# Optimization experiments

Measured on AMD Instinct MI355X. Metric: run time of the kernel, lower is better.

Reference implementation:

```python
import jax, jax.numpy as jnp
import numpy as np

K = 20          # neighbors
EPS = 1e-5      # BatchNorm eps
SLOPE = 0.2     # LeakyReLU negative slope


def setup_inputs() -> dict:
    key = jax.random.key(0)
    ks = jax.random.split(key, 6)
    B, C, N, O = 8, 3, 4096, 64
    x = jax.random.normal(ks[0], (B, C, N), dtype=jnp.float32)
    W = jax.random.normal(ks[1], (O, 2 * C), dtype=jnp.float32) * 0.1  # conv1x1 weight, bias=False
    gamma = 1.0 + 0.1 * jax.random.normal(ks[2], (O,), dtype=jnp.float32)
    beta = 0.1 * jax.random.normal(ks[3], (O,), dtype=jnp.float32)
    mean = 0.1 * jax.random.normal(ks[4], (O,), dtype=jnp.float32)
    var = jax.random.uniform(ks[5], (O,), dtype=jnp.float32, minval=0.5, maxval=1.5)
    return {"x": x, "W": W, "gamma": gamma, "beta": beta, "mean": mean, "var": var}


def reference(x, W, gamma, beta, mean, var):
    # x: [B, C, N]
    B, C, N = x.shape
    xt = jnp.swapaxes(x, 1, 2)                                   # [B, N, C]
    xx = jnp.sum(x * x, axis=1)                                  # [B, N]
    pd = 2.0 * jnp.einsum('bnc,bmc->bnm', xt, xt) - xx[:, :, None] - xx[:, None, :]
    _, idx = jax.lax.top_k(pd, K)                                # [B, N, K] nearest neighbors
    # gather neighbor features per batch
    feat = jax.vmap(lambda f, i: f[i])(xt, idx)                  # [B, N, K, C]
    center = xt[:, :, None, :]                                   # [B, N, 1, C]
    edge = jnp.concatenate(
        [feat - center, jnp.broadcast_to(center, feat.shape)], axis=-1)  # [B, N, K, 2C]
    # 1x1 conv == channel matmul
    y = jnp.einsum('bnkc,oc->bnko', edge, W)                     # [B, N, K, O]
    inv = gamma / jnp.sqrt(var + EPS)                            # fused inference BatchNorm
    y = y * inv + (beta - mean * inv)
    y = jnp.where(y >= 0, y, SLOPE * y)                          # LeakyReLU(0.2)
    y = jnp.max(y, axis=2)                                       # max over k -> [B, N, O]
    return jnp.swapaxes(y, 1, 2)                                 # [B, O, N]
```

## Files before the change

kernel.cpp:

```cpp
#include <hip/hip_runtime.h>
#include <math.h>

#define NPTS 4096
#define KNN  20
#define NOUT 64
#define QPB  8
#define BLKT (QPB * 64)
#define PCAP 128
#define HALF 2048

__device__ __forceinline__ unsigned ord32(float f) {
    unsigned u = __float_as_uint(f);
    int m = ((int)u) >> 31;
    return u ^ ((unsigned)m | 0x80000000u);
}

__device__ __forceinline__ int mbcnt64(unsigned long long m) {
    return __builtin_amdgcn_mbcnt_hi((unsigned)(m >> 32),
           __builtin_amdgcn_mbcnt_lo((unsigned)m, 0));
}

__global__ __launch_bounds__(256) void pack_kernel(const float* __restrict__ x,
                                                   float4* __restrict__ xq) {
    const int i = blockIdx.x * 256 + threadIdx.x;
    const int b = i >> 12, j = i & (NPTS - 1);
    const float* xb = x + (size_t)b * 3 * NPTS;
    const float a0 = xb[j], a1 = xb[NPTS + j], a2 = xb[2 * NPTS + j];
    xq[i] = make_float4(a0, a1, a2, -fmaf(a0, a0, fmaf(a1, a1, a2 * a2)));
}

__global__ __launch_bounds__(BLKT, 6) void edgeconv_kernel(
    const float4* __restrict__ xq,
    const float* __restrict__ Wm,
    const float* __restrict__ gamma,
    const float* __restrict__ beta,
    const float* __restrict__ mean,
    const float* __restrict__ var,
    float* __restrict__ out)
{
    const int bid = blockIdx.x;
    const int b   = bid >> 9;
    const int n0  = (bid & 511) * QPB;
    const int t    = threadIdx.x;
    const int lane = t & 63;
    const int w    = t >> 6;

    __shared__ float4 tile[HALF];
    __shared__ unsigned long long pool[QPB * PCAP];
    __shared__ unsigned idxs[QPB][KNN];
    __shared__ float outT[NOUT * 9];
    __shared__ int cnt[QPB];

    const float4* xqb = xq + (size_t)b * NPTS;

    if (lane == 0) cnt[w] = 0;

    #pragma unroll
    for (int k2 = 0; k2 < HALF / BLKT; ++k2) {
        const int c = t + k2 * BLKT;
        tile[c] = xqb[c];
    }
    __syncthreads();

    const int nu = __builtin_amdgcn_readfirstlane(n0 + w);
    const float4 pv = xqb[nu];
    const float q0 = 2.f * pv.x, q1 = 2.f * pv.y, q2 = 2.f * pv.z;

    float vmax = -INFINITY;
    #pragma unroll
    for (int g = 0; g < 4; ++g) {
        float4 cc[8];
        #pragma unroll
        for (int u = 0; u < 8; ++u) cc[u] = tile[(g * 8 + u) * 64 + lane];
        #pragma unroll
        for (int u = 0; u < 8; ++u) {
            const float e = fmaf(q0, cc[u].x, fmaf(q1, cc[u].y, fmaf(q2, cc[u].z, cc[u].w)));
            vmax = fmaxf(vmax, e);
        }
    }

    float T;
    {
        float v = vmax;
        #pragma unroll
        for (int k = 2; k <= 64; k <<= 1) {
            #pragma unroll
            for (int j = k >> 1; j > 0; j >>= 1) {
                const float o = __shfl_xor(v, j, 64);
                const bool keep_min = ((lane & j) == 0) == ((lane & k) != 0);
                v = keep_min ? fminf(v, o) : fmaxf(v, o);
            }
        }
        T = __shfl(v, 19, 64);
    }

    const int invl = (NPTS - 1) - lane;
    #pragma unroll
    for (int g = 0; g < 4; ++g) {
        float4 cc[8];
        #pragma unroll
        for (int u = 0; u < 8; ++u) cc[u] = tile[(g * 8 + u) * 64 + lane];
        #pragma unroll
        for (int u = 0; u < 8; ++u) {
            const float e = fmaf(q0, cc[u].x, fmaf(q1, cc[u].y, fmaf(q2, cc[u].z, cc[u].w)));
            if (e >= T) {
                const int pos = atomicAdd(&cnt[w], 1);
                if (pos < PCAP)
                    pool[w * PCAP + pos] =
                        ((unsigned long long)ord32(e) << 32) |
                        (unsigned)(invl - (g * 8 + u) * 64);
            }
        }
    }

    #pragma unroll
    for (int g = 4; g < 8; ++g) {
        float4 cc[8];
        #pragma unroll
        for (int u = 0; u < 8; ++u) cc[u] = xqb[(g * 8 + u) * 64 + lane];
        #pragma unroll
        for (int u = 0; u < 8; ++u) {
            const float e = fmaf(q0, cc[u].x, fmaf(q1, cc[u].y, fmaf(q2, cc[u].z, cc[u].w)));
            if (e >= T) {
                const int pos = atomicAdd(&cnt[w], 1);
                if (pos < PCAP)
                    pool[w * PCAP + pos] =
                        ((unsigned long long)ord32(e) << 32) |
                        (unsigned)(invl - (g * 8 + u) * 64);
            }
        }
    }

    const int cntw = __builtin_amdgcn_readfirstlane(cnt[w]);
    const int cnt_ = (cntw < PCAP) ? cntw : PCAP;

    unsigned long long kk = 0ull;
    if (lane < cnt_) kk = pool[w * PCAP + lane];

    if (cnt_ <= 64) {
        const unsigned key = (unsigned)(kk >> 32);
        unsigned v = key;
        #pragma unroll
        for (int k = 2; k <= 64; k <<= 1) {
            #pragma unroll
            for (int j = k >> 1; j > 0; j >>= 1) {
                const unsigned o = (unsigned)__shfl_xor((int)v, j, 64);
                const bool keep_min = ((lane & j) == 0) == ((lane & k) != 0);
                v = keep_min ? min(v, o) : max(v, o);
            }
        }
        const unsigned K20 = (unsigned)__shfl((int)v, 19, 64);
        const unsigned long long ge = __ballot(key >= K20);
        if (__popcll(ge) == KNN) {
            if (key >= K20) idxs[w][mbcnt64(ge)] = (unsigned)kk;
        } else {
            unsigned long long key64 = kk;
            #pragma unroll
            for (int k = 2; k <= 64; k <<= 1) {
                #pragma unroll
                for (int j = k >> 1; j > 0; j >>= 1) {
                    const unsigned long long o = __shfl_xor(key64, j, 64);
                    const bool keep_min = ((lane & j) == 0) == ((lane & k) != 0);
                    const unsigned long long mn = (key64 < o) ? key64 : o;
                    const unsigned long long mx = (key64 < o) ? o : key64;
                    key64 = keep_min ? mn : mx;
                }
            }
            if (lane < KNN) idxs[w][lane] = (unsigned)key64;
        }
    } else {
        for (int r = 0; r < KNN; ++r) {
            unsigned long long bk = 0ull; int bp = -1;
            for (int i = lane; i < cnt_; i += 64) {
                const unsigned long long e = pool[w * PCAP + i];
                if (e > bk) { bk = e; bp = i; }
            }
            unsigned long long rb = bk;
            #pragma unroll
            for (int s = 32; s > 0; s >>= 1) {
                const unsigned long long o = __shfl_xor(rb, s, 64);
                if (o > rb) rb = o;
            }
            if (bk == rb && bp >= 0) pool[w * PCAP + bp] = 0ull;
            if (lane == 0) idxs[w][r] = (unsigned)rb;
        }
    }

    const unsigned myidx = idxs[w][(lane < KNN) ? lane : 0];

    const int o = lane;
    const float iv   = gamma[o] / sqrtf(var[o] + 1e-5f);
    const float bias = beta[o] - mean[o] * iv;
    const float* Wr = Wm + o * 6;
    const float w0p = Wr[0] * iv, w1p = Wr[1] * iv, w2p = Wr[2] * iv;
    const float w3p = Wr[3] * iv, w4p = Wr[4] * iv, w5p = Wr[5] * iv;
    const float basep = fmaf(w3p, pv.x, fmaf(w4p, pv.y, fmaf(w5p, pv.z, bias)));
    const float base2 = basep - fmaf(w0p, pv.x, fmaf(w1p, pv.y, w2p * pv.z));

    float best = -INFINITY;
    #pragma unroll
    for (int k = 0; k < KNN; ++k) {
        const int lk = __builtin_amdgcn_readlane((int)myidx, k);
        const int gi = __builtin_amdgcn_readfirstlane((NPTS - 1) - lk);
        const float4 f = xqb[gi];
        float y = fmaf(w0p, f.x, fmaf(w1p, f.y, fmaf(w2p, f.z, base2)));
        y = fmaxf(y, 0.2f * y);
        best = fmaxf(best, y);
    }

    outT[o * 9 + w] = best;
    __syncthreads();

    if (t < NOUT * 2) {
        const int oo = t >> 1, seg = t & 1;
        const int sb = oo * 9 + seg * 4;
        float4 vv;
        vv.x = outT[sb + 0]; vv.y = outT[sb + 1];
        vv.z = outT[sb + 2]; vv.w = outT[sb + 3];
        *(float4*)(out + ((size_t)b * NOUT + oo) * NPTS + n0 + seg * 4) = vv;
    }
}

extern "C" void kernel_launch(void* const* d_in, const int* in_sizes, int n_in,
                              void* d_out, int out_size, void* d_ws, size_t ws_size,
                              hipStream_t stream) {
    const float* x     = (const float*)d_in[0];
    const float* Wm    = (const float*)d_in[1];
    const float* gamma = (const float*)d_in[2];
    const float* beta  = (const float*)d_in[3];
    const float* mean  = (const float*)d_in[4];
    const float* var   = (const float*)d_in[5];
    float* out = (float*)d_out;
    float4* xq = (float4*)d_ws;

    const int B = in_sizes[0] / (3 * NPTS);
    pack_kernel<<<B * NPTS / 256, 256, 0, stream>>>(x, xq);
    const int nblocks = B * (NPTS / QPB);
    edgeconv_kernel<<<nblocks, BLKT, 0, stream>>>(xq, Wm, gamma, beta, mean, var, out);
}
```

Before: 150.8 us.

## Process two queries per wavefront to reuse candidate point loads

Each wavefront now computes distances for two query points against the same loaded candidate points, doubling queries per block and halving block count. This amortizes LDS and global loads of the point cloud across two queries. It raises register pressure under the existing launch bounds and shrinks the per-query candidate pool capacity to fit shared memory.

```diff
diff --git a/kernel.cpp b/kernel.cpp
--- a/kernel.cpp
+++ b/kernel.cpp
@@ -4,9 +4,11 @@
 #define NPTS 4096
 #define KNN  20
 #define NOUT 64
-#define QPB  8
-#define BLKT (QPB * 64)
-#define PCAP 128
+#define WPB  8
+#define QPW  2
+#define QBLK (WPB * QPW)
+#define BLKT (WPB * 64)
+#define PCAP 96
 #define HALF 2048
 
 __device__ __forceinline__ unsigned ord32(float f) {
@@ -39,21 +41,21 @@
     float* __restrict__ out)
 {
     const int bid = blockIdx.x;
-    const int b   = bid >> 9;
-    const int n0  = (bid & 511) * QPB;
+    const int b   = bid >> 8;
+    const int n0  = (bid & 255) * QBLK;
     const int t    = threadIdx.x;
     const int lane = t & 63;
     const int w    = t >> 6;
 
     __shared__ float4 tile[HALF];
-    __shared__ unsigned long long pool[QPB * PCAP];
-    __shared__ unsigned idxs[QPB][KNN];
-    __shared__ float outT[NOUT * 9];
-    __shared__ int cnt[QPB];
+    __shared__ unsigned long long pool[QBLK * PCAP];
+    __shared__ unsigned idxs[QBLK][KNN];
+    __shared__ float outT[NOUT * (QBLK + 1)];
+    __shared__ int cnt[QBLK];
 
     const float4* xqb = xq + (size_t)b * NPTS;
 
-    if (lane == 0) cnt[w] = 0;
+    if (lane < QPW) cnt[QPW * w + lane] = 0;
 
     #pragma unroll
     for (int k2 = 0; k2 < HALF / BLKT; ++k2) {
@@ -62,11 +64,14 @@
     }
     __syncthreads();
 
-    const int nu = __builtin_amdgcn_readfirstlane(n0 + w);
-    const float4 pv = xqb[nu];
-    const float q0 = 2.f * pv.x, q1 = 2.f * pv.y, q2 = 2.f * pv.z;
-
-    float vmax = -INFINITY;
+    const int na = __builtin_amdgcn_readfirstlane(n0 + QPW * w);
+    const int nb = na + 1;
+    const float4 pva = xqb[na];
+    const float4 pvb = xqb[nb];
+    const float qa0 = 2.f * pva.x, qa1 = 2.f * pva.y, qa2 = 2.f * pva.z;
+    const float qb0 = 2.f * pvb.x, qb1 = 2.f * pvb.y, qb2 = 2.f * pvb.z;
+
+    float vma = -INFINITY, vmb = -INFINITY;
     #pragma unroll
     for (int g = 0; g < 4; ++g) {
         float4 cc[8];
@@ -74,27 +79,37 @@
         for (int u = 0; u < 8; ++u) cc[u] = tile[(g * 8 + u) * 64 + lane];
         #pragma unroll
         for (int u = 0; u < 8; ++u) {
-            const float e = fmaf(q0, cc[u].x, fmaf(q1, cc[u].y, fmaf(q2, cc[u].z, cc[u].w)));
-            vmax = fmaxf(vmax, e);
-        }
-    }
-
-    float T;
+            const float ea = fmaf(qa0, cc[u].x, fmaf(qa1, cc[u].y, fmaf(qa2, cc[u].z, cc[u].w)));
+            const float eb = fmaf(qb0, cc[u].x, fmaf(qb1, cc[u].y, fmaf(qb2, cc[u].z, cc[u].w)));
+            vma = fmaxf(vma, ea);
+            vmb = fmaxf(vmb, eb);
+        }
+    }
+
+    float Ta, Tb;
     {
-        float v = vmax;
+        float va = vma, vb = vmb;
         #pragma unroll
         for (int k = 2; k <= 64; k <<= 1) {
             #pragma unroll
             for (int j = k >> 1; j > 0; j >>= 1) {
-                const float o = __shfl_xor(v, j, 64);
+                const float oa = __shfl_xor(va, j, 64);
+                const float ob = __shfl_xor(vb, j, 64);
                 const bool keep_min = ((lane & j) == 0) == ((lane & k) != 0);
-                v = keep_min ? fminf(v, o) : fmaxf(v, o);
-            }
-        }
-        T = __shfl(v, 19, 64);
+                va = keep_min ? fminf(va, oa) : fmaxf(va, oa);
+                vb = keep_min ? fminf(vb, ob) : fmaxf(vb, ob);
+            }
+        }
+        Ta = __shfl(va, 19, 64);
+        Tb = __shfl(vb, 19, 64);
     }
 
     const int invl = (NPTS - 1) - lane;
+    int* cnta = &cnt[QPW * w];
+    int* cntb = &cnt[QPW * w + 1];
+    unsigned long long* poola = pool + (QPW * w) * PCAP;
+    unsigned long long* poolb = pool + (QPW * w + 1) * PCAP;
+
     #pragma unroll
     for (int g = 0; g < 4; ++g) {
         float4 cc[8];
@@ -102,13 +117,18 @@
         for (int u = 0; u < 8; ++u) cc[u] = tile[(g * 8 + u) * 64 + lane];
         #pragma unroll
         for (int u = 0; u < 8; ++u) {
-            const float e = fmaf(q0, cc[u].x, fmaf(q1, cc[u].y, fmaf(q2, cc[u].z, cc[u].w)));
-            if (e >= T) {
-                const int pos = atomicAdd(&cnt[w], 1);
-                if (pos < PCAP)
-                    pool[w * PCAP + pos] =
-                        ((unsigned long long)ord32(e) << 32) |
-                        (unsigned)(invl - (g * 8 + u) * 64);
+            const float ea = fmaf(qa0, cc[u].x, fmaf(qa1, cc[u].y, fmaf(qa2, cc[u].z, cc[u].w)));
+            const float eb = fmaf(qb0, cc[u].x, fmaf(qb1, cc[u].y, fmaf(qb2, cc[u].z, cc[u].w)));
+            const unsigned tag = (unsigned)(invl - (g * 8 + u) * 64);
+            if (ea >= Ta) {
+                const int pos = atomicAdd(cnta, 1);
+                if (pos < PCAP)
+                    poola[pos] = ((unsigned long long)ord32(ea) << 32) | tag;
+            }
+            if (eb >= Tb) {
+                const int pos = atomicAdd(cntb, 1);
+                if (pos < PCAP)
+                    poolb[pos] = ((unsigned long long)ord32(eb) << 32) | tag;
             }
         }
     }
@@ -120,73 +140,84 @@
         for (int u = 0; u < 8; ++u) cc[u] = xqb[(g * 8 + u) * 64 + lane];
         #pragma unroll
         for (int u = 0; u < 8; ++u) {
-            const float e = fmaf(q0, cc[u].x, fmaf(q1, cc[u].y, fmaf(q2, cc[u].z, cc[u].w)));
-            if (e >= T) {
-                const int pos = atomicAdd(&cnt[w], 1);
-                if (pos < PCAP)
-                    pool[w * PCAP + pos] =
-                        ((unsigned long long)ord32(e) << 32) |
-                        (unsigned)(invl - (g * 8 + u) * 64);
-            }
-        }
-    }
-
-    const int cntw = __builtin_amdgcn_readfirstlane(cnt[w]);
-    const int cnt_ = (cntw < PCAP) ? cntw : PCAP;
-
-    unsigned long long kk = 0ull;
-    if (lane < cnt_) kk = pool[w * PCAP + lane];
-
-    if (cnt_ <= 64) {
-        const unsigned key = (unsigned)(kk >> 32);
-        unsigned v = key;
-        #pragma unroll
-        for (int k = 2; k <= 64; k <<= 1) {
-            #pragma unroll
-            for (int j = k >> 1; j > 0; j >>= 1) {
-                const unsigned o = (unsigned)__shfl_xor((int)v, j, 64);
-                const bool keep_min = ((lane & j) == 0) == ((lane & k) != 0);
-                v = keep_min ? min(v, o) : max(v, o);
-            }
-        }
-        const unsigned K20 = (unsigned)__shfl((int)v, 19, 64);
-        const unsigned long long ge = __ballot(key >= K20);
-        if (__popcll(ge) == KNN) {
-            if (key >= K20) idxs[w][mbcnt64(ge)] = (unsigned)kk;
-        } else {
-            unsigned long long key64 = kk;
+            const float ea = fmaf(qa0, cc[u].x, fmaf(qa1, cc[u].y, fmaf(qa2, cc[u].z, cc[u].w)));
+            const float eb = fmaf(qb0, cc[u].x, fmaf(qb1, cc[u].y, fmaf(qb2, cc[u].z, cc[u].w)));
+            const unsigned tag = (unsigned)(invl - (g * 8 + u) * 64);
+            if (ea >= Ta) {
+                const int pos = atomicAdd(cnta, 1);
+                if (pos < PCAP)
+                    poola[pos] = ((unsigned long long)ord32(ea) << 32) | tag;
+            }
+            if (eb >= Tb) {
+                const int pos = atomicAdd(cntb, 1);
+                if (pos < PCAP)
+                    poolb[pos] = ((unsigned long long)ord32(eb) << 32) | tag;
+            }
+        }
+    }
+
+    #pragma unroll
+    for (int q = 0; q < QPW; ++q) {
+        const int pr = QPW * w + q;
+        unsigned long long* pl = pool + (size_t)pr * PCAP;
+        const int cntw = __builtin_amdgcn_readfirstlane(cnt[pr]);
+        const int cnt_ = (cntw < PCAP) ? cntw : PCAP;
+
+        unsigned long long kk = 0ull;
+        if (lane < cnt_) kk = pl[lane];
+
+        if (cnt_ <= 64) {
+            const unsigned key = (unsigned)(kk >> 32);
+            unsigned v = key;
             #pragma unroll
             for (int k = 2; k <= 64; k <<= 1) {
                 #pragma unroll
                 for (int j = k >> 1; j > 0; j >>= 1) {
-                    const unsigned long long o = __shfl_xor(key64, j, 64);
+                    const unsigned o = (unsigned)__shfl_xor((int)v, j, 64);
                     const bool keep_min = ((lane & j) == 0) == ((lane & k) != 0);
-                    const unsigned long long mn = (key64 < o) ? key64 : o;
-                    const unsigned long long mx = (key64 < o) ? o : key64;
-                    key64 = keep_min ? mn : mx;
-                }
-            }
-            if (lane < KNN) idxs[w][lane] = (unsigned)key64;
-        }
-    } else {
-        for (int r = 0; r < KNN; ++r) {
-            unsigned long long bk = 0ull; int bp = -1;
-            for (int i = lane; i < cnt_; i += 64) {
-                const unsigned long long e = pool[w * PCAP + i];
-                if (e > bk) { bk = e; bp = i; }
-            }
-            unsigned long long rb = bk;
-            #pragma unroll
-            for (int s = 32; s > 0; s >>= 1) {
-                const unsigned long long o = __shfl_xor(rb, s, 64);
-                if (o > rb) rb = o;
-            }
-            if (bk == rb && bp >= 0) pool[w * PCAP + bp] = 0ull;
-            if (lane == 0) idxs[w][r] = (unsigned)rb;
-        }
-    }
-
-    const unsigned myidx = idxs[w][(lane < KNN) ? lane : 0];
+                    v = keep_min ? min(v, o) : max(v, o);
+                }
+            }
+            const unsigned K20 = (unsigned)__shfl((int)v, 19, 64);
+            const unsigned long long ge = __ballot(key >= K20);
+            if (__popcll(ge) == KNN) {
+                if (key >= K20) idxs[pr][mbcnt64(ge)] = (unsigned)kk;
+            } else {
+                unsigned long long key64 = kk;
+                #pragma unroll
+                for (int k = 2; k <= 64; k <<= 1) {
+                    #pragma unroll
+                    for (int j = k >> 1; j > 0; j >>= 1) {
+                        const unsigned long long o = __shfl_xor(key64, j, 64);
+                        const bool keep_min = ((lane & j) == 0) == ((lane & k) != 0);
+                        const unsigned long long mn = (key64 < o) ? key64 : o;
+                        const unsigned long long mx = (key64 < o) ? o : key64;
+                        key64 = keep_min ? mn : mx;
+                    }
+                }
+                if (lane < KNN) idxs[pr][lane] = (unsigned)key64;
+            }
+        } else {
+            for (int r = 0; r < KNN; ++r) {
+                unsigned long long bk = 0ull; int bp = -1;
+                for (int i = lane; i < cnt_; i += 64) {
+                    const unsigned long long e = pl[i];
+                    if (e > bk) { bk = e; bp = i; }
+                }
+                unsigned long long rb = bk;
+                #pragma unroll
+                for (int s = 32; s > 0; s >>= 1) {
+                    const unsigned long long o = __shfl_xor(rb, s, 64);
+                    if (o > rb) rb = o;
+                }
+                if (bk == rb && bp >= 0) pl[bp] = 0ull;
+                if (lane == 0) idxs[pr][r] = (unsigned)rb;
+            }
+        }
+    }
+
+    const unsigned myidxa = idxs[QPW * w][(lane < KNN) ? lane : 0];
+    const unsigned myidxb = idxs[QPW * w + 1][(lane < KNN) ? lane : 0];
 
     const int o = lane;
     const float iv   = gamma[o] / sqrtf(var[o] + 1e-5f);
@@ -194,26 +225,35 @@
     const float* Wr = Wm + o * 6;
     const float w0p = Wr[0] * iv, w1p = Wr[1] * iv, w2p = Wr[2] * iv;
     const float w3p = Wr[3] * iv, w4p = Wr[4] * iv, w5p = Wr[5] * iv;
-    const float basep = fmaf(w3p, pv.x, fmaf(w4p, pv.y, fmaf(w5p, pv.z, bias)));
-    const float base2 = basep - fmaf(w0p, pv.x, fmaf(w1p, pv.y, w2p * pv.z));
-
-    float best = -INFINITY;
+    const float basea = fmaf(w3p, pva.x, fmaf(w4p, pva.y, fmaf(w5p, pva.z, bias)));
+    const float base2a = basea - fmaf(w0p, pva.x, fmaf(w1p, pva.y, w2p * pva.z));
+    const float baseb = fmaf(w3p, pvb.x, fmaf(w4p, pvb.y, fmaf(w5p, pvb.z, bias)));
+    const float base2b = baseb - fmaf(w0p, pvb.x, fmaf(w1p, pvb.y, w2p * pvb.z));
+
+    float besta = -INFINITY, bestb = -INFINITY;
     #pragma unroll
     for (int k = 0; k < KNN; ++k) {
-        const int lk = __builtin_amdgcn_readlane((int)myidx, k);
-        const int gi = __builtin_amdgcn_readfirstlane((NPTS - 1) - lk);
-        const float4 f = xqb[gi];
-        float y = fmaf(w0p, f.x, fmaf(w1p, f.y, fmaf(w2p, f.z, base2)));
-        y = fmaxf(y, 0.2f * y);
-        best = fmaxf(best, y);
-    }
-
-    outT[o * 9 + w] = best;
+        const int lka = __builtin_amdgcn_readlane((int)myidxa, k);
+        const int lkb = __builtin_amdgcn_readlane((int)myidxb, k);
+        const int gia = __builtin_amdgcn_readfirstlane((NPTS - 1) - lka);
+        const int gib = __builtin_amdgcn_readfirstlane((NPTS - 1) - lkb);
+        const float4 fa = xqb[gia];
+        const float4 fb = xqb[gib];
+        float ya = fmaf(w0p, fa.x, fmaf(w1p, fa.y, fmaf(w2p, fa.z, base2a)));
+        float yb = fmaf(w0p, fb.x, fmaf(w1p, fb.y, fmaf(w2p, fb.z, base2b)));
+        ya = fmaxf(ya, 0.2f * ya);
+        yb = fmaxf(yb, 0.2f * yb);
+        besta = fmaxf(besta, ya);
+        bestb = fmaxf(bestb, yb);
+    }
+
+    outT[o * (QBLK + 1) + QPW * w]     = besta;
+    outT[o * (QBLK + 1) + QPW * w + 1] = bestb;
     __syncthreads();
 
-    if (t < NOUT * 2) {
-        const int oo = t >> 1, seg = t & 1;
-        const int sb = oo * 9 + seg * 4;
+    if (t < NOUT * 4) {
+        const int oo = t >> 2, seg = t & 3;
+        const int sb = oo * (QBLK + 1) + seg * 4;
         float4 vv;
         vv.x = outT[sb + 0]; vv.y = outT[sb + 1];
         vv.z = outT[sb + 2]; vv.w = outT[sb + 3];
@@ -235,6 +275,6 @@
 
     const int B = in_sizes[0] / (3 * NPTS);
     pack_kernel<<<B * NPTS / 256, 256, 0, stream>>>(x, xq);
-    const int nblocks = B * (NPTS / QPB);
+    const int nblocks = B * (NPTS / QBLK);
     edgeconv_kernel<<<nblocks, BLKT, 0, stream>>>(xq, Wm, gamma, beta, mean, var, out);
 }
```

Measured after the change: 144.2 us. -4.4%, faster.
